# Performance work log

Measured on AMD Instinct MI355X. Metric: run time of the kernel, lower is better.

## Reference

```python
import jax, jax.numpy as jnp
import numpy as np

N_NODES = 100000
IN_F = 128
H_F = 128
LOOKBACK = 3
N_EDGES = 640000


def setup_inputs() -> dict:
    key = jax.random.key(0)
    ks = jax.random.split(key, 16)
    s = lambda k, shp: jax.random.normal(k, shp, dtype=jnp.float32) * 0.05
    inp = {
        "feat": jax.random.normal(ks[0], (N_NODES, IN_F), dtype=jnp.float32),
        "edges": jax.random.randint(ks[1], (LOOKBACK, 2, N_EDGES), 0, N_NODES, dtype=jnp.int32),
        # conv1 (SAGEConv pool, in->h) params
        "Wp1": s(ks[2], (IN_F, IN_F)), "bp1": jnp.zeros((IN_F,), jnp.float32),
        "Ws1": s(ks[3], (H_F, IN_F)), "Wn1": s(ks[4], (H_F, IN_F)), "b1": jnp.zeros((H_F,), jnp.float32),
        # BatchNorm1d affine params (training-mode batch stats)
        "gamma": jnp.ones((H_F,), jnp.float32), "beta": jnp.zeros((H_F,), jnp.float32),
        # conv2 (SAGEConv pool, h->h) params
        "Wp2": s(ks[5], (H_F, H_F)), "bp2": jnp.zeros((H_F,), jnp.float32),
        "Ws2": s(ks[6], (H_F, H_F)), "Wn2": s(ks[7], (H_F, H_F)), "b2": jnp.zeros((H_F,), jnp.float32),
    }
    return inp


def _sage_pool_conv(h, src, dst, Wp, bp, Ws, Wn, b):
    # pool aggregator: m = relu(fc_pool(h)); neigh = max over in-edges
    m = jax.nn.relu(h @ Wp.T + bp)                      # [N, d]
    agg = jax.ops.segment_max(m[src], dst, num_segments=N_NODES)  # [N, d]
    agg = jnp.where(jnp.isfinite(agg), agg, 0.0)        # nodes with no in-edges -> 0
    return h @ Ws.T + agg @ Wn.T + b


def _batchnorm(x, gamma, beta, eps=1e-5):
    mu = jnp.mean(x, axis=0)
    var = jnp.var(x, axis=0)
    return (x - mu) * jax.lax.rsqrt(var + eps) * gamma + beta


def reference(feat, edges, Wp1, bp1, Ws1, Wn1, b1, gamma, beta, Wp2, bp2, Ws2, Wn2, b2):
    def per_graph(e):
        src, dst = e[0], e[1]
        h = _sage_pool_conv(feat, src, dst, Wp1, bp1, Ws1, Wn1, b1)
        h = _batchnorm(h, gamma, beta)
        h = jax.nn.relu(h)
        h = _sage_pool_conv(h, src, dst, Wp2, bp2, Ws2, Wn2, b2)
        return h

    return jax.vmap(per_graph)(edges)  # [lookback, N, H_F]
```

## Files before the change

### kernel.cpp

```cpp
#include <hip/hip_runtime.h>
#include <hip/hip_bf16.h>

#define NNODES 100000
#define FD 128
#define NEDGES 640000
#define NB 391
#define GRID1 1564
#define OFFS_U32 100032
#define BNRED 64

typedef __bf16 bf16x8 __attribute__((ext_vector_type(8)));
typedef __bf16 bf16x4 __attribute__((ext_vector_type(4)));
typedef float f32x4 __attribute__((ext_vector_type(4)));
typedef unsigned short u16x8 __attribute__((ext_vector_type(8)));

__device__ __forceinline__ bf16x8 cvt8(float4 a, float4 b) {
  bf16x8 r;
  r[0] = (__bf16)a.x; r[1] = (__bf16)a.y; r[2] = (__bf16)a.z; r[3] = (__bf16)a.w;
  r[4] = (__bf16)b.x; r[5] = (__bf16)b.y; r[6] = (__bf16)b.z; r[7] = (__bf16)b.w;
  return r;
}

__global__ __launch_bounds__(256) void packw6_k(
    const float* __restrict__ W0, const float* __restrict__ W1,
    const float* __restrict__ W2, const float* __restrict__ W3,
    const float* __restrict__ W4, const float* __restrict__ W5,
    __bf16* __restrict__ out) {
  const int gidx = blockIdx.x * 256 + threadIdx.x;
  const int wi = gidx >> 11;
  const int f = gidx & 2047;
  const float* W = wi == 0 ? W0 : wi == 1 ? W1 : wi == 2 ? W2
                 : wi == 3 ? W3 : wi == 4 ? W4 : W5;
  const int c = f >> 8, kk = (f >> 6) & 3, lane = f & 63;
  const int lr = lane & 15, lg = lane >> 4;
  const float* p = W + (c * 16 + lr) * FD + kk * 32 + lg * 8;
  *(bf16x8*)(out + (long)gidx * 8) = cvt8(*(const float4*)p, *(const float4*)(p + 4));
}

template <int AM>
__device__ __forceinline__ void load_arow(const void* __restrict__ A, long row,
                                          int kbase, const float* __restrict__ scsh,
                                          bf16x8 (&af)[4]) {
  if constexpr (AM == 1) {
#pragma unroll
    for (int kk = 0; kk < 4; ++kk)
      af[kk] = *(const bf16x8*)((const __bf16*)A + row * FD + kbase + kk * 32);
  } else if constexpr (AM == 3) {
#pragma unroll
    for (int kk = 0; kk < 4; ++kk) {
      const int k = kbase + kk * 32;
      const bf16x8 r = *(const bf16x8*)((const __bf16*)A + row * FD + k);
      const float4 scx = *(const float4*)(scsh + k);
      const float4 scy = *(const float4*)(scsh + k + 4);
      const float4 shx = *(const float4*)(scsh + 128 + k);
      const float4 shy = *(const float4*)(scsh + 128 + k + 4);
      bf16x8 o;
      o[0] = (__bf16)fmaxf((float)r[0] * scx.x + shx.x, 0.f);
      o[1] = (__bf16)fmaxf((float)r[1] * scx.y + shx.y, 0.f);
      o[2] = (__bf16)fmaxf((float)r[2] * scx.z + shx.z, 0.f);
      o[3] = (__bf16)fmaxf((float)r[3] * scx.w + shx.w, 0.f);
      o[4] = (__bf16)fmaxf((float)r[4] * scy.x + shy.x, 0.f);
      o[5] = (__bf16)fmaxf((float)r[5] * scy.y + shy.y, 0.f);
      o[6] = (__bf16)fmaxf((float)r[6] * scy.z + shy.z, 0.f);
      o[7] = (__bf16)fmaxf((float)r[7] * scy.w + shy.w, 0.f);
      af[kk] = o;
    }
  } else {
#pragma unroll
    for (int kk = 0; kk < 4; ++kk) {
      const int k = kbase + kk * 32;
      const float* ap = (const float*)A + row * FD + k;
      af[kk] = cvt8(*(const float4*)ap, *(const float4*)(ap + 4));
    }
  }
}

template <int A0M, int A1M, bool TWOA, bool RELU, bool OUTBF16, bool STATS, bool WRITEB>
__global__ __launch_bounds__(256, 4) void gemm_k(
    const void* __restrict__ A0, long a0s, const void* __restrict__ A1, long a1s,
    const __bf16* __restrict__ W0p, const __bf16* __restrict__ W1p,
    const float* __restrict__ bias, const float* __restrict__ scsh0,
    void* __restrict__ outp, long os, float* __restrict__ pblk,
    __bf16* __restrict__ bcopy, int M) {
  const int g = blockIdx.y;
  const int wid = threadIdx.x >> 6;
  const int rw = wid & 1;
  const int cw = wid >> 1;
  const int lane = threadIdx.x & 63;
  const int lr = lane & 15;
  const int lg = lane >> 4;
  const int kbase = lg * 8;
  const int rbase = blockIdx.x * 64 + rw * 32;
  __shared__ float s_red[2][4][64];

  const void* A0g = (const char*)A0 + (long)g * a0s;
  const void* A1g = (const char*)A1 + (TWOA ? (long)g * a1s : 0);
  void* outg = (char*)outp + (long)g * os;
  const float* scshg = (A0M == 3 || A1M == 3) ? scsh0 + (long)g * 256 : nullptr;
  float* pblkg = STATS ? pblk + (long)g * ((long)GRID1 * 256) : nullptr;

  if constexpr (!STATS) {
    if (rbase >= M) return;
  }

  f32x4 acc[2][4];
#pragma unroll
  for (int t = 0; t < 2; ++t)
#pragma unroll
    for (int c = 0; c < 4; ++c) acc[t][c] = (f32x4){0.f, 0.f, 0.f, 0.f};

  {
    bf16x8 a0[2][4];
#pragma unroll
    for (int t = 0; t < 2; ++t) {
      long row = rbase + t * 16 + lr;
      if (row > M - 1) row = M - 1;
      load_arow<A0M>(A0g, row, kbase, scshg, a0[t]);
    }
    if constexpr (WRITEB) {
      if (cw == 0) {
#pragma unroll
        for (int t = 0; t < 2; ++t) {
          const int row = rbase + t * 16 + lr;
          if (row < M)
#pragma unroll
            for (int kk = 0; kk < 4; ++kk)
              *(bf16x8*)(bcopy + (long)row * FD + kbase + kk * 32) = a0[t][kk];
        }
      }
    }
#pragma unroll
    for (int c = 0; c < 4; ++c) {
      bf16x8 bw[4];
#pragma unroll
      for (int kk = 0; kk < 4; ++kk)
        bw[kk] = *(const bf16x8*)(W0p + ((long)(((cw * 4 + c) * 4 + kk) * 64 + lane)) * 8);
#pragma unroll
      for (int t = 0; t < 2; ++t)
#pragma unroll
        for (int kk = 0; kk < 4; ++kk)
          acc[t][c] = __builtin_amdgcn_mfma_f32_16x16x32_bf16(bw[kk], a0[t][kk], acc[t][c], 0, 0, 0);
    }
  }
  if constexpr (TWOA) {
    bf16x8 a1[2][4];
#pragma unroll
    for (int t = 0; t < 2; ++t) {
      long row = rbase + t * 16 + lr;
      if (row > M - 1) row = M - 1;
      load_arow<A1M>(A1g, row, kbase, scshg, a1[t]);
    }
#pragma unroll
    for (int c = 0; c < 4; ++c) {
      bf16x8 bw[4];
#pragma unroll
      for (int kk = 0; kk < 4; ++kk)
        bw[kk] = *(const bf16x8*)(W1p + ((long)(((cw * 4 + c) * 4 + kk) * 64 + lane)) * 8);
#pragma unroll
      for (int t = 0; t < 2; ++t)
#pragma unroll
        for (int kk = 0; kk < 4; ++kk)
          acc[t][c] = __builtin_amdgcn_mfma_f32_16x16x32_bf16(bw[kk], a1[t][kk], acc[t][c], 0, 0, 0);
    }
  }

  float ps[4][4], pss[4][4];
  if constexpr (STATS) {
#pragma unroll
    for (int c = 0; c < 4; ++c)
#pragma unroll
      for (int j = 0; j < 4; ++j) { ps[c][j] = 0.f; pss[c][j] = 0.f; }
  }

#pragma unroll
  for (int t = 0; t < 2; ++t) {
    const int row = rbase + t * 16 + lr;
    const bool ok = row < M;
#pragma unroll
    for (int c = 0; c < 4; ++c) {
      const int cb = cw * 64 + c * 16 + lg * 4;
      f32x4 v = acc[t][c];
      if (bias) {
        const float4 bv = *(const float4*)(bias + cb);
        v[0] += bv.x; v[1] += bv.y; v[2] += bv.z; v[3] += bv.w;
      }
      if constexpr (STATS) {
        if (ok) {
#pragma unroll
          for (int j = 0; j < 4; ++j) { ps[c][j] += v[j]; pss[c][j] += v[j] * v[j]; }
        }
      }
      if constexpr (RELU) {
#pragma unroll
        for (int j = 0; j < 4; ++j) v[j] = fmaxf(v[j], 0.f);
      }
      if (ok) {
        if constexpr (OUTBF16) {
          bf16x4 o;
          o[0] = (__bf16)v[0]; o[1] = (__bf16)v[1];
          o[2] = (__bf16)v[2]; o[3] = (__bf16)v[3];
          *(bf16x4*)((__bf16*)outg + (long)row * FD + cb) = o;
        } else {
          *(f32x4*)((float*)outg + (long)row * FD + cb) = v;
        }
      }
    }
  }

  if constexpr (STATS) {
#pragma unroll
    for (int c = 0; c < 4; ++c)
#pragma unroll
      for (int j = 0; j < 4; ++j) {
        float s = ps[c][j], q = pss[c][j];
        s += __shfl_xor(s, 1); s += __shfl_xor(s, 2);
        s += __shfl_xor(s, 4); s += __shfl_xor(s, 8);
        q += __shfl_xor(q, 1); q += __shfl_xor(q, 2);
        q += __shfl_xor(q, 4); q += __shfl_xor(q, 8);
        if (lr == 0) {
          s_red[0][wid][c * 16 + lg * 4 + j] = s;
          s_red[1][wid][c * 16 + lg * 4 + j] = q;
        }
      }
    __syncthreads();
    const int tid = threadIdx.x;
    const int wh = tid >> 7, cg = tid & 127;
    const int cwi = cg >> 6, cl = cg & 63;
    pblkg[(long)blockIdx.x * 256 + tid] =
        s_red[wh][cwi * 2 + 0][cl] + s_red[wh][cwi * 2 + 1][cl];
  }
}

__global__ __launch_bounds__(256) void bn_red1_k(const float* __restrict__ pblk,
                                                 float* __restrict__ pblk2) {
  const int g = blockIdx.y;
  const float* p = pblk + (long)g * GRID1 * 256;
  float s = 0.f;
  for (int r = blockIdx.x; r < GRID1; r += BNRED) s += p[(long)r * 256 + threadIdx.x];
  pblk2[((long)g * BNRED + blockIdx.x) * 256 + threadIdx.x] = s;
}

__global__ __launch_bounds__(256) void bn_final2_k(const float* __restrict__ pblk2,
                                                   const float* __restrict__ gamma,
                                                   const float* __restrict__ beta,
                                                   float* __restrict__ scsh3) {
  __shared__ float s_ss[128];
  const int g = blockIdx.y;
  const int tid = threadIdx.x;
  const float* p = pblk2 + (long)g * BNRED * 256;
  float s = 0.f;
#pragma unroll
  for (int r = 0; r < BNRED; ++r) s += p[r * 256 + tid];
  if (tid >= 128) s_ss[tid - 128] = s;
  __syncthreads();
  if (tid < 128) {
    const float mu = s / (float)NNODES;
    const float var = s_ss[tid] / (float)NNODES - mu * mu;
    const float sc = rsqrtf(var + 1e-5f) * gamma[tid];
    scsh3[g * 256 + tid] = sc;
    scsh3[g * 256 + 128 + tid] = beta[tid] - mu * sc;
  }
}


__global__ __launch_bounds__(256) void hist_rank3_k(const int* __restrict__ edges,
                                                    unsigned* __restrict__ deg3,
                                                    unsigned short* __restrict__ rank3) {
  const int g = blockIdx.y;
  const int e = blockIdx.x * 256 + threadIdx.x;
  if (e < NEDGES) {
    const int d = edges[(long)g * 2 * NEDGES + NEDGES + e];
    const unsigned r = atomicAdd(&deg3[(long)g * NNODES + d], 1u);
    rank3[(long)g * NEDGES + e] = (unsigned short)r;
  }
}

__global__ __launch_bounds__(256) void blocksum3_k(const unsigned* __restrict__ deg3,
                                                   unsigned* __restrict__ bsum3) {
  __shared__ unsigned s[256];
  const int g = blockIdx.y;
  const int i = blockIdx.x * 256 + threadIdx.x;
  s[threadIdx.x] = (i < NNODES) ? deg3[(long)g * NNODES + i] : 0u;
  __syncthreads();
#pragma unroll
  for (int o = 128; o > 0; o >>= 1) {
    if (threadIdx.x < o) s[threadIdx.x] += s[threadIdx.x + o];
    __syncthreads();
  }
  if (threadIdx.x == 0) bsum3[g * NB + blockIdx.x] = s[0];
}

__global__ __launch_bounds__(512) void scanb3_k(const unsigned* __restrict__ bsum3,
                                                unsigned* __restrict__ boffs3,
                                                unsigned* __restrict__ offs3) {
  __shared__ unsigned s[512];
  const int g = blockIdx.y;
  const unsigned v = (threadIdx.x < NB) ? bsum3[g * NB + threadIdx.x] : 0u;
  s[threadIdx.x] = v;
  __syncthreads();
#pragma unroll
  for (int o = 1; o < 512; o <<= 1) {
    unsigned t = (threadIdx.x >= o) ? s[threadIdx.x - o] : 0u;
    __syncthreads();
    s[threadIdx.x] += t;
    __syncthreads();
  }
  if (threadIdx.x < NB) boffs3[g * NB + threadIdx.x] = s[threadIdx.x] - v;
  if (threadIdx.x == 0) offs3[(long)g * OFFS_U32 + NNODES] = NEDGES;
}

__global__ __launch_bounds__(256) void offsets3_k(const unsigned* __restrict__ deg3,
                                                  const unsigned* __restrict__ boffs3,
                                                  unsigned* __restrict__ offs3) {
  __shared__ unsigned s[256];
  const int g = blockIdx.y;
  const int i = blockIdx.x * 256 + threadIdx.x;
  const unsigned v = (i < NNODES) ? deg3[(long)g * NNODES + i] : 0u;
  s[threadIdx.x] = v;
  __syncthreads();
#pragma unroll
  for (int o = 1; o < 256; o <<= 1) {
    unsigned t = (threadIdx.x >= o) ? s[threadIdx.x - o] : 0u;
    __syncthreads();
    s[threadIdx.x] += t;
    __syncthreads();
  }
  const unsigned excl = s[threadIdx.x] - v + boffs3[g * NB + blockIdx.x];
  if (i < NNODES) offs3[(long)g * OFFS_U32 + i] = excl;
}

__global__ __launch_bounds__(256) void scat3_k(const int* __restrict__ edges,
                                               const unsigned* __restrict__ offs3,
                                               const unsigned short* __restrict__ rank3,
                                               int* __restrict__ ssrc3) {
  const int g = blockIdx.y;
  const int e = blockIdx.x * 256 + threadIdx.x;
  if (e < NEDGES) {
    const int s = edges[(long)g * 2 * NEDGES + e];
    const int d = edges[(long)g * 2 * NEDGES + NEDGES + e];
    const unsigned p = offs3[(long)g * OFFS_U32 + d] + rank3[(long)g * NEDGES + e];
    ssrc3[(long)g * NEDGES + p] = s;
  }
}

__global__ __launch_bounds__(256) void agg_k(const unsigned short* __restrict__ m,
                                             long ms, const int* __restrict__ ssrc3,
                                             const unsigned* __restrict__ offs3,
                                             unsigned short* __restrict__ agg3) {
  const int g = blockIdx.y;
  const unsigned short* mg = m + (long)g * ms;
  const int* ssrc = ssrc3 + (long)g * NEDGES;
  const unsigned* offs = offs3 + (long)g * OFFS_U32;
  unsigned short* agg = agg3 + (long)g * NNODES * FD;

  const int gid = blockIdx.x * 256 + threadIdx.x;
  const int node = gid >> 4;
  if (node >= NNODES) return;
  const int fl = (gid & 15) * 8;
  const unsigned beg = offs[node], end = offs[node + 1];
  u16x8 acc = {0, 0, 0, 0, 0, 0, 0, 0};
  unsigned i = beg;
  for (; i + 2 <= end; i += 2) {
    const int s0 = ssrc[i];
    const int s1 = ssrc[i + 1];
    const u16x8 v0 = *(const u16x8*)(mg + (long)s0 * FD + fl);
    const u16x8 v1 = *(const u16x8*)(mg + (long)s1 * FD + fl);
#pragma unroll
    for (int j = 0; j < 8; ++j) {
      const unsigned short mx = v0[j] > v1[j] ? v0[j] : v1[j];
      acc[j] = mx > acc[j] ? mx : acc[j];
    }
  }
  if (i < end) {
    const u16x8 v = *(const u16x8*)(mg + (long)ssrc[i] * FD + fl);
#pragma unroll
    for (int j = 0; j < 8; ++j) acc[j] = v[j] > acc[j] ? v[j] : acc[j];
  }
  *(u16x8*)(agg + (long)node * FD + fl) = acc;
}

__global__ __launch_bounds__(256) void zero_k(float4* __restrict__ p, long n4) {
  const long i = (long)blockIdx.x * 256 + threadIdx.x;
  if (i < n4) p[i] = (float4){0.f, 0.f, 0.f, 0.f};
}

extern "C" void kernel_launch(void* const* d_in, const int* in_sizes, int n_in,
                              void* d_out, int out_size, void* d_ws, size_t ws_size,
                              hipStream_t stream) {
  const float* feat = (const float*)d_in[0];
  const int* edges = (const int*)d_in[1];
  const float* Wp1 = (const float*)d_in[2];
  const float* bp1 = (const float*)d_in[3];
  const float* Ws1 = (const float*)d_in[4];
  const float* Wn1 = (const float*)d_in[5];
  const float* b1 = (const float*)d_in[6];
  const float* gamma = (const float*)d_in[7];
  const float* beta = (const float*)d_in[8];
  const float* Wp2 = (const float*)d_in[9];
  const float* bp2 = (const float*)d_in[10];
  const float* Ws2 = (const float*)d_in[11];
  const float* Wn2 = (const float*)d_in[12];
  const float* b2 = (const float*)d_in[13];

  const long SZ_BF = 25600000;
  const long SZ_F32 = 51200000;

  char* w = (char*)d_ws;
  __bf16* m1 = (__bf16*)w;
  __bf16* featb = (__bf16*)(w + 25600000);
  __bf16* h1b3 = (__bf16*)(w + 51200000);
  __bf16* aggb3 = (__bf16*)(w + 128000000);
  __bf16* m2_3 = (__bf16*)(w + 204800000);
  float* pblk3 = (float*)(w + 204800000);
  float* pblk2_3 = (float*)(w + 209604608);
  __bf16* wpk = (__bf16*)(w + 281600000);
  float* scsh3 = (float*)(w + 281796608);
  unsigned* deg3 = (unsigned*)(w + 281799680);
  unsigned* offs3 = (unsigned*)(w + 282999680);
  unsigned* bsum3 = (unsigned*)(w + 284200064);
  unsigned* boffs3 = (unsigned*)(w + 284204928);
  unsigned short* rank3 = (unsigned short*)(w + 284209792);
  int* ssrc3 = (int*)(w + 288049792);

  __bf16* Wp1p = wpk;
  __bf16* Ws1p = wpk + 16384;
  __bf16* Wn1p = wpk + 2 * 16384;
  __bf16* Wp2p = wpk + 3 * 16384;
  __bf16* Ws2p = wpk + 4 * 16384;
  __bf16* Wn2p = wpk + 5 * 16384;

  const dim3 blk(256);
  const int edgeGrid = (NEDGES + 255) / 256;
  const int aggGrid = (NNODES * 16 + 255) / 256;
  const int degZeroGrid = (3 * NNODES / 4 + 255) / 256;

  packw6_k<<<48, blk, 0, stream>>>(Wp1, Ws1, Wn1, Wp2, Ws2, Wn2, wpk);

  zero_k<<<degZeroGrid, blk, 0, stream>>>((float4*)deg3, 3L * NNODES / 4);
  hist_rank3_k<<<dim3(edgeGrid, 3), blk, 0, stream>>>(edges, deg3, rank3);
  blocksum3_k<<<dim3(NB, 3), blk, 0, stream>>>(deg3, bsum3);
  scanb3_k<<<dim3(1, 3), dim3(512), 0, stream>>>(bsum3, boffs3, offs3);
  offsets3_k<<<dim3(NB, 3), blk, 0, stream>>>(deg3, boffs3, offs3);
  scat3_k<<<dim3(edgeGrid, 3), blk, 0, stream>>>(edges, offs3, rank3, ssrc3);

  gemm_k<0, 0, false, true, true, false, true><<<dim3(GRID1, 1), blk, 0, stream>>>(
      feat, 0, nullptr, 0, Wp1p, nullptr, bp1, nullptr, m1, 0, nullptr, featb, NNODES);

  agg_k<<<dim3(aggGrid, 3), blk, 0, stream>>>((const unsigned short*)m1, 0L,
                                              ssrc3, offs3, (unsigned short*)aggb3);
  gemm_k<1, 1, true, false, true, true, false><<<dim3(GRID1, 3), blk, 0, stream>>>(
      aggb3, SZ_BF, featb, 0, Wn1p, Ws1p, b1, nullptr, h1b3, SZ_BF, pblk3, nullptr, NNODES);
  bn_red1_k<<<dim3(BNRED, 3), blk, 0, stream>>>(pblk3, pblk2_3);
  bn_final2_k<<<dim3(1, 3), blk, 0, stream>>>(pblk2_3, gamma, beta, scsh3);

  gemm_k<3, 0, false, true, true, false, false><<<dim3(GRID1, 3), blk, 0, stream>>>(
      h1b3, SZ_BF, nullptr, 0, Wp2p, nullptr, bp2, scsh3, m2_3, SZ_BF, nullptr, nullptr, NNODES);
  agg_k<<<dim3(aggGrid, 3), blk, 0, stream>>>((const unsigned short*)m2_3,
                                              (long)NNODES * FD, ssrc3, offs3,
                                              (unsigned short*)aggb3);
  gemm_k<3, 1, true, false, false, false, false><<<dim3(GRID1, 3), blk, 0, stream>>>(
      h1b3, SZ_BF, aggb3, SZ_BF, Ws2p, Wn2p, b2, scsh3, d_out, SZ_F32, nullptr, nullptr, NNODES);
}
```

Baseline: 569.2 us.

## Make GEMM persistent with register-resident weights and parallelize aggregation per wavefront

The GEMM kernel becomes a grid-stride loop over 32-row chunks. Each wave loads its 32-column slice of the packed weights into registers once and reuses them across chunks, instead of reloading weights in every 64-row block. The BN partial-stats buffer shrinks to match the smaller grid and moves to a separate workspace region. The aggregation kernel now assigns one wavefront per node, with four edge groups splitting the in-edges, and merges their partial maxima with cross-lane shuffles. This adds edge-level parallelism for high-degree nodes, at the cost of idle lanes on low-degree nodes and extra shuffle work.

Result: slower. 660.6 us (+16.1%).

```diff
diff --git a/kernel.cpp b/kernel.cpp
--- a/kernel.cpp
+++ b/kernel.cpp
@@ -5,7 +5,8 @@
 #define FD 128
 #define NEDGES 640000
 #define NB 391
-#define GRID1 1564
+#define NCHK 3125
+#define GXC 625
 #define OFFS_U32 100032
 #define BNRED 64
 
@@ -76,132 +77,117 @@
 }
 
 template <int A0M, int A1M, bool TWOA, bool RELU, bool OUTBF16, bool STATS, bool WRITEB>
-__global__ __launch_bounds__(256, 4) void gemm_k(
+__global__ __launch_bounds__(256) void gemm_k(
     const void* __restrict__ A0, long a0s, const void* __restrict__ A1, long a1s,
     const __bf16* __restrict__ W0p, const __bf16* __restrict__ W1p,
     const float* __restrict__ bias, const float* __restrict__ scsh0,
     void* __restrict__ outp, long os, float* __restrict__ pblk,
-    __bf16* __restrict__ bcopy, int M) {
+    __bf16* __restrict__ bcopy) {
   const int g = blockIdx.y;
   const int wid = threadIdx.x >> 6;
-  const int rw = wid & 1;
-  const int cw = wid >> 1;
   const int lane = threadIdx.x & 63;
   const int lr = lane & 15;
   const int lg = lane >> 4;
   const int kbase = lg * 8;
-  const int rbase = blockIdx.x * 64 + rw * 32;
-  __shared__ float s_red[2][4][64];
+  __shared__ float s_red[2][4][32];
 
   const void* A0g = (const char*)A0 + (long)g * a0s;
   const void* A1g = (const char*)A1 + (TWOA ? (long)g * a1s : 0);
   void* outg = (char*)outp + (long)g * os;
   const float* scshg = (A0M == 3 || A1M == 3) ? scsh0 + (long)g * 256 : nullptr;
-  float* pblkg = STATS ? pblk + (long)g * ((long)GRID1 * 256) : nullptr;
-
-  if constexpr (!STATS) {
-    if (rbase >= M) return;
-  }
-
-  f32x4 acc[2][4];
-#pragma unroll
-  for (int t = 0; t < 2; ++t)
-#pragma unroll
-    for (int c = 0; c < 4; ++c) acc[t][c] = (f32x4){0.f, 0.f, 0.f, 0.f};
-
-  {
+
+  bf16x8 bw0[2][4], bw1[2][4];
+#pragma unroll
+  for (int ci = 0; ci < 2; ++ci)
+#pragma unroll
+    for (int kk = 0; kk < 4; ++kk) {
+      const long f = ((long)((wid * 2 + ci) * 4 + kk) * 64 + lane) * 8;
+      bw0[ci][kk] = *(const bf16x8*)(W0p + f);
+      if constexpr (TWOA) bw1[ci][kk] = *(const bf16x8*)(W1p + f);
+    }
+
+  float ps[2][4], pss[2][4];
+  if constexpr (STATS) {
+#pragma unroll
+    for (int ci = 0; ci < 2; ++ci)
+#pragma unroll
+      for (int j = 0; j < 4; ++j) { ps[ci][j] = 0.f; pss[ci][j] = 0.f; }
+  }
+
+  for (int ch = blockIdx.x; ch < NCHK; ch += GXC) {
+    const int rbase = ch * 32;
     bf16x8 a0[2][4];
 #pragma unroll
+    for (int t = 0; t < 2; ++t)
+      load_arow<A0M>(A0g, (long)(rbase + t * 16 + lr), kbase, scshg, a0[t]);
+    bf16x8 a1[2][4];
+    if constexpr (TWOA) {
+#pragma unroll
+      for (int t = 0; t < 2; ++t)
+        load_arow<A1M>(A1g, (long)(rbase + t * 16 + lr), kbase, scshg, a1[t]);
+    }
+
+    f32x4 acc[2][2];
+#pragma unroll
+    for (int t = 0; t < 2; ++t)
+#pragma unroll
+      for (int ci = 0; ci < 2; ++ci) acc[t][ci] = (f32x4){0.f, 0.f, 0.f, 0.f};
+
+#pragma unroll
+    for (int ci = 0; ci < 2; ++ci)
+#pragma unroll
+      for (int t = 0; t < 2; ++t)
+#pragma unroll
+        for (int kk = 0; kk < 4; ++kk)
+          acc[t][ci] = __builtin_amdgcn_mfma_f32_16x16x32_bf16(bw0[ci][kk], a0[t][kk], acc[t][ci], 0, 0, 0);
+    if constexpr (TWOA) {
+#pragma unroll
+      for (int ci = 0; ci < 2; ++ci)
+#pragma unroll
+        for (int t = 0; t < 2; ++t)
+#pragma unroll
+          for (int kk = 0; kk < 4; ++kk)
+            acc[t][ci] = __builtin_amdgcn_mfma_f32_16x16x32_bf16(bw1[ci][kk], a1[t][kk], acc[t][ci], 0, 0, 0);
+    }
+
+    if constexpr (WRITEB) {
+      if (wid == 0) {
+#pragma unroll
+        for (int t = 0; t < 2; ++t) {
+          const long row = rbase + t * 16 + lr;
+#pragma unroll
+          for (int kk = 0; kk < 4; ++kk)
+            *(bf16x8*)(bcopy + row * FD + kbase + kk * 32) = a0[t][kk];
+        }
+      }
+    }
+
+#pragma unroll
     for (int t = 0; t < 2; ++t) {
-      long row = rbase + t * 16 + lr;
-      if (row > M - 1) row = M - 1;
-      load_arow<A0M>(A0g, row, kbase, scshg, a0[t]);
-    }
-    if constexpr (WRITEB) {
-      if (cw == 0) {
-#pragma unroll
-        for (int t = 0; t < 2; ++t) {
-          const int row = rbase + t * 16 + lr;
-          if (row < M)
-#pragma unroll
-            for (int kk = 0; kk < 4; ++kk)
-              *(bf16x8*)(bcopy + (long)row * FD + kbase + kk * 32) = a0[t][kk];
-        }
-      }
-    }
-#pragma unroll
-    for (int c = 0; c < 4; ++c) {
-      bf16x8 bw[4];
-#pragma unroll
-      for (int kk = 0; kk < 4; ++kk)
-        bw[kk] = *(const bf16x8*)(W0p + ((long)(((cw * 4 + c) * 4 + kk) * 64 + lane)) * 8);
-#pragma unroll
-      for (int t = 0; t < 2; ++t)
-#pragma unroll
-        for (int kk = 0; kk < 4; ++kk)
-          acc[t][c] = __builtin_amdgcn_mfma_f32_16x16x32_bf16(bw[kk], a0[t][kk], acc[t][c], 0, 0, 0);
-    }
-  }
-  if constexpr (TWOA) {
-    bf16x8 a1[2][4];
-#pragma unroll
-    for (int t = 0; t < 2; ++t) {
-      long row = rbase + t * 16 + lr;
-      if (row > M - 1) row = M - 1;
-      load_arow<A1M>(A1g, row, kbase, scshg, a1[t]);
-    }
-#pragma unroll
-    for (int c = 0; c < 4; ++c) {
-      bf16x8 bw[4];
-#pragma unroll
-      for (int kk = 0; kk < 4; ++kk)
-        bw[kk] = *(const bf16x8*)(W1p + ((long)(((cw * 4 + c) * 4 + kk) * 64 + lane)) * 8);
-#pragma unroll
-      for (int t = 0; t < 2; ++t)
-#pragma unroll
-        for (int kk = 0; kk < 4; ++kk)
-          acc[t][c] = __builtin_amdgcn_mfma_f32_16x16x32_bf16(bw[kk], a1[t][kk], acc[t][c], 0, 0, 0);
-    }
-  }
-
-  float ps[4][4], pss[4][4];
-  if constexpr (STATS) {
-#pragma unroll
-    for (int c = 0; c < 4; ++c)
-#pragma unroll
-      for (int j = 0; j < 4; ++j) { ps[c][j] = 0.f; pss[c][j] = 0.f; }
-  }
-
-#pragma unroll
-  for (int t = 0; t < 2; ++t) {
-    const int row = rbase + t * 16 + lr;
-    const bool ok = row < M;
-#pragma unroll
-    for (int c = 0; c < 4; ++c) {
-      const int cb = cw * 64 + c * 16 + lg * 4;
-      f32x4 v = acc[t][c];
-      if (bias) {
-        const float4 bv = *(const float4*)(bias + cb);
-        v[0] += bv.x; v[1] += bv.y; v[2] += bv.z; v[3] += bv.w;
-      }
-      if constexpr (STATS) {
-        if (ok) {
-#pragma unroll
-          for (int j = 0; j < 4; ++j) { ps[c][j] += v[j]; pss[c][j] += v[j] * v[j]; }
-        }
-      }
-      if constexpr (RELU) {
-#pragma unroll
-        for (int j = 0; j < 4; ++j) v[j] = fmaxf(v[j], 0.f);
-      }
-      if (ok) {
+      const long row = rbase + t * 16 + lr;
+#pragma unroll
+      for (int ci = 0; ci < 2; ++ci) {
+        const int cb = wid * 32 + ci * 16 + lg * 4;
+        f32x4 v = acc[t][ci];
+        if (bias) {
+          const float4 bv = *(const float4*)(bias + cb);
+          v[0] += bv.x; v[1] += bv.y; v[2] += bv.z; v[3] += bv.w;
+        }
+        if constexpr (STATS) {
+#pragma unroll
+          for (int j = 0; j < 4; ++j) { ps[ci][j] += v[j]; pss[ci][j] += v[j] * v[j]; }
+        }
+        if constexpr (RELU) {
+#pragma unroll
+          for (int j = 0; j < 4; ++j) v[j] = fmaxf(v[j], 0.f);
+        }
         if constexpr (OUTBF16) {
           bf16x4 o;
           o[0] = (__bf16)v[0]; o[1] = (__bf16)v[1];
           o[2] = (__bf16)v[2]; o[3] = (__bf16)v[3];
-          *(bf16x4*)((__bf16*)outg + (long)row * FD + cb) = o;
+          *(bf16x4*)((__bf16*)outg + row * FD + cb) = o;
         } else {
-          *(f32x4*)((float*)outg + (long)row * FD + cb) = v;
+          *(f32x4*)((float*)outg + row * FD + cb) = v;
         }
       }
     }
@@ -209,34 +195,33 @@
 
   if constexpr (STATS) {
 #pragma unroll
-    for (int c = 0; c < 4; ++c)
+    for (int ci = 0; ci < 2; ++ci)
 #pragma unroll
       for (int j = 0; j < 4; ++j) {
-        float s = ps[c][j], q = pss[c][j];
+        float s = ps[ci][j], q = pss[ci][j];
         s += __shfl_xor(s, 1); s += __shfl_xor(s, 2);
         s += __shfl_xor(s, 4); s += __shfl_xor(s, 8);
         q += __shfl_xor(q, 1); q += __shfl_xor(q, 2);
         q += __shfl_xor(q, 4); q += __shfl_xor(q, 8);
         if (lr == 0) {
-          s_red[0][wid][c * 16 + lg * 4 + j] = s;
-          s_red[1][wid][c * 16 + lg * 4 + j] = q;
+          s_red[0][wid][ci * 16 + lg * 4 + j] = s;
+          s_red[1][wid][ci * 16 + lg * 4 + j] = q;
         }
       }
     __syncthreads();
     const int tid = threadIdx.x;
-    const int wh = tid >> 7, cg = tid & 127;
-    const int cwi = cg >> 6, cl = cg & 63;
-    pblkg[(long)blockIdx.x * 256 + tid] =
-        s_red[wh][cwi * 2 + 0][cl] + s_red[wh][cwi * 2 + 1][cl];
+    const int which = tid >> 7, col = tid & 127;
+    float* pblkg = pblk + (long)g * ((long)GXC * 256);
+    pblkg[(long)blockIdx.x * 256 + tid] = s_red[which][col >> 5][col & 31];
   }
 }
 
 __global__ __launch_bounds__(256) void bn_red1_k(const float* __restrict__ pblk,
                                                  float* __restrict__ pblk2) {
   const int g = blockIdx.y;
-  const float* p = pblk + (long)g * GRID1 * 256;
+  const float* p = pblk + (long)g * GXC * 256;
   float s = 0.f;
-  for (int r = blockIdx.x; r < GRID1; r += BNRED) s += p[(long)r * 256 + threadIdx.x];
+  for (int r = blockIdx.x; r < GXC; r += BNRED) s += p[(long)r * 256 + threadIdx.x];
   pblk2[((long)g * BNRED + blockIdx.x) * 256 + threadIdx.x] = s;
 }
 
@@ -353,18 +338,17 @@
   const unsigned* offs = offs3 + (long)g * OFFS_U32;
   unsigned short* agg = agg3 + (long)g * NNODES * FD;
 
-  const int gid = blockIdx.x * 256 + threadIdx.x;
-  const int node = gid >> 4;
-  if (node >= NNODES) return;
-  const int fl = (gid & 15) * 8;
+  const int node = blockIdx.x * 4 + (threadIdx.x >> 6);
+  const int lane = threadIdx.x & 63;
+  const int eg = lane >> 4;
+  const int fl = (lane & 15) * 8;
   const unsigned beg = offs[node], end = offs[node + 1];
+
   u16x8 acc = {0, 0, 0, 0, 0, 0, 0, 0};
-  unsigned i = beg;
-  for (; i + 2 <= end; i += 2) {
-    const int s0 = ssrc[i];
-    const int s1 = ssrc[i + 1];
-    const u16x8 v0 = *(const u16x8*)(mg + (long)s0 * FD + fl);
-    const u16x8 v1 = *(const u16x8*)(mg + (long)s1 * FD + fl);
+  unsigned i = beg + eg;
+  for (; i + 4 < end; i += 8) {
+    const u16x8 v0 = *(const u16x8*)(mg + (long)ssrc[i] * FD + fl);
+    const u16x8 v1 = *(const u16x8*)(mg + (long)ssrc[i + 4] * FD + fl);
 #pragma unroll
     for (int j = 0; j < 8; ++j) {
       const unsigned short mx = v0[j] > v1[j] ? v0[j] : v1[j];
@@ -376,7 +360,23 @@
 #pragma unroll
     for (int j = 0; j < 8; ++j) acc[j] = v[j] > acc[j] ? v[j] : acc[j];
   }
-  *(u16x8*)(agg + (long)node * FD + fl) = acc;
+
+  int4 a = __builtin_bit_cast(int4, acc);
+#pragma unroll
+  for (int mask = 16; mask <= 32; mask <<= 1) {
+    int4 o;
+    o.x = __shfl_xor(a.x, mask);
+    o.y = __shfl_xor(a.y, mask);
+    o.z = __shfl_xor(a.z, mask);
+    o.w = __shfl_xor(a.w, mask);
+    u16x8 A = __builtin_bit_cast(u16x8, a);
+    const u16x8 O = __builtin_bit_cast(u16x8, o);
+#pragma unroll
+    for (int j = 0; j < 8; ++j) A[j] = O[j] > A[j] ? O[j] : A[j];
+    a = __builtin_bit_cast(int4, A);
+  }
+  if (eg == 0)
+    *(u16x8*)(agg + (long)node * FD + fl) = __builtin_bit_cast(u16x8, a);
 }
 
 __global__ __launch_bounds__(256) void zero_k(float4* __restrict__ p, long n4) {
@@ -411,8 +411,6 @@
   __bf16* h1b3 = (__bf16*)(w + 51200000);
   __bf16* aggb3 = (__bf16*)(w + 128000000);
   __bf16* m2_3 = (__bf16*)(w + 204800000);
-  float* pblk3 = (float*)(w + 204800000);
-  float* pblk2_3 = (float*)(w + 209604608);
   __bf16* wpk = (__bf16*)(w + 281600000);
   float* scsh3 = (float*)(w + 281796608);
   unsigned* deg3 = (unsigned*)(w + 281799680);
@@ -421,6 +419,8 @@
   unsigned* boffs3 = (unsigned*)(w + 284204928);
   unsigned short* rank3 = (unsigned short*)(w + 284209792);
   int* ssrc3 = (int*)(w + 288049792);
+  float* pblk3 = (float*)(w + 295729792);
+  float* pblk2_3 = (float*)(w + 297649792);
 
   __bf16* Wp1p = wpk;
   __bf16* Ws1p = wpk + 16384;
@@ -431,7 +431,6 @@
 
   const dim3 blk(256);
   const int edgeGrid = (NEDGES + 255) / 256;
-  const int aggGrid = (NNODES * 16 + 255) / 256;
   const int degZeroGrid = (3 * NNODES / 4 + 255) / 256;
 
   packw6_k<<<48, blk, 0, stream>>>(Wp1, Ws1, Wn1, Wp2, Ws2, Wn2, wpk);
@@ -443,21 +442,21 @@
   offsets3_k<<<dim3(NB, 3), blk, 0, stream>>>(deg3, boffs3, offs3);
   scat3_k<<<dim3(edgeGrid, 3), blk, 0, stream>>>(edges, offs3, rank3, ssrc3);
 
-  gemm_k<0, 0, false, true, true, false, true><<<dim3(GRID1, 1), blk, 0, stream>>>(
-      feat, 0, nullptr, 0, Wp1p, nullptr, bp1, nullptr, m1, 0, nullptr, featb, NNODES);
-
-  agg_k<<<dim3(aggGrid, 3), blk, 0, stream>>>((const unsigned short*)m1, 0L,
-                                              ssrc3, offs3, (unsigned short*)aggb3);
-  gemm_k<1, 1, true, false, true, true, false><<<dim3(GRID1, 3), blk, 0, stream>>>(
-      aggb3, SZ_BF, featb, 0, Wn1p, Ws1p, b1, nullptr, h1b3, SZ_BF, pblk3, nullptr, NNODES);
+  gemm_k<0, 0, false, true, true, false, true><<<dim3(GXC, 1), blk, 0, stream>>>(
+      feat, 0, nullptr, 0, Wp1p, nullptr, bp1, nullptr, m1, 0, nullptr, featb);
+
+  agg_k<<<dim3(25000, 3), blk, 0, stream>>>((const unsigned short*)m1, 0L,
+                                            ssrc3, offs3, (unsigned short*)aggb3);
+  gemm_k<1, 1, true, false, true, true, false><<<dim3(GXC, 3), blk, 0, stream>>>(
+      aggb3, SZ_BF, featb, 0, Wn1p, Ws1p, b1, nullptr, h1b3, SZ_BF, pblk3, nullptr);
   bn_red1_k<<<dim3(BNRED, 3), blk, 0, stream>>>(pblk3, pblk2_3);
   bn_final2_k<<<dim3(1, 3), blk, 0, stream>>>(pblk2_3, gamma, beta, scsh3);
 
-  gemm_k<3, 0, false, true, true, false, false><<<dim3(GRID1, 3), blk, 0, stream>>>(
-      h1b3, SZ_BF, nullptr, 0, Wp2p, nullptr, bp2, scsh3, m2_3, SZ_BF, nullptr, nullptr, NNODES);
-  agg_k<<<dim3(aggGrid, 3), blk, 0, stream>>>((const unsigned short*)m2_3,
-                                              (long)NNODES * FD, ssrc3, offs3,
-                                              (unsigned short*)aggb3);
-  gemm_k<3, 1, true, false, false, false, false><<<dim3(GRID1, 3), blk, 0, stream>>>(
-      h1b3, SZ_BF, aggb3, SZ_BF, Ws2p, Wn2p, b2, scsh3, d_out, SZ_F32, nullptr, nullptr, NNODES);
-}
+  gemm_k<3, 0, false, true, true, false, false><<<dim3(GXC, 3), blk, 0, stream>>>(
+      h1b3, SZ_BF, nullptr, 0, Wp2p, nullptr, bp2, scsh3, m2_3, SZ_BF, nullptr, nullptr);
+  agg_k<<<dim3(25000, 3), blk, 0, stream>>>((const unsigned short*)m2_3,
+                                            (long)NNODES * FD, ssrc3, offs3,
+                                            (unsigned short*)aggb3);
+  gemm_k<3, 1, true, false, false, false, false><<<dim3(GXC, 3), blk, 0, stream>>>(
+      h1b3, SZ_BF, aggb3, SZ_BF, Ws2p, Wn2p, b2, scsh3, d_out, SZ_F32, nullptr, nullptr);
+}
```
